# Kernel tuning notes

Measured on AMD Instinct MI355X. Metric: run time of the kernel, lower is better.

Reference implementation:

```python
import jax, jax.numpy as jnp
import numpy as np

H = 512   # embedding_dim (forced by Attention(512,512))
F = 21    # n_features
T = 28    # output_length

def _cell(x, h, c, Wih, Whh, b):
    # PyTorch LSTMCell math, gate order i,f,g,o
    g = x @ Wih.T + h @ Whh.T + b
    i, f, gg, o = jnp.split(g, 4, axis=-1)
    c2 = jax.nn.sigmoid(f) * c + jax.nn.sigmoid(i) * jnp.tanh(gg)
    h2 = jax.nn.sigmoid(o) * jnp.tanh(c2)
    return h2, c2

def _lstm3(inp, h, c, Wih0, Wih1, Wih2, Whh, bih, bhh):
    # 3-layer LSTM, single time step. h,c: [3,1,H]
    Wihs = (Wih0, Wih1, Wih2)
    hs, cs = [], []
    x = inp
    for l in range(3):
        hl, cl = _cell(x, h[l], c[l], Wihs[l], Whh[l], bih[l] + bhh[l])
        hs.append(hl); cs.append(cl)
        x = hl
    return x, jnp.stack(hs), jnp.stack(cs)

def setup_inputs() -> dict:
    key = jax.random.key(0)
    ks = jax.random.split(key, 20)
    s = 0.05
    f32 = jnp.float32
    return {
        "x": jax.random.normal(ks[0], (1, F), f32),
        "prev_y": jax.random.normal(ks[1], (1, F), f32),
        "enc_Wih0": jax.random.normal(ks[2], (4*H, F), f32) * s,
        "enc_Wih1": jax.random.normal(ks[3], (4*H, H), f32) * s,
        "enc_Wih2": jax.random.normal(ks[4], (4*H, H), f32) * s,
        "enc_Whh": jax.random.normal(ks[5], (3, 4*H, H), f32) * s,
        "enc_bih": jax.random.normal(ks[6], (3, 4*H), f32) * s,
        "enc_bhh": jax.random.normal(ks[7], (3, 4*H), f32) * s,
        "attn_W": jax.random.normal(ks[8], (H, 2*H), f32) * s,
        "attn_b": jax.random.normal(ks[9], (H,), f32) * s,
        "v_W": jax.random.normal(ks[10], (1, H), f32) * s,
        "dec_Wih0": jax.random.normal(ks[11], (4*H, H+F), f32) * s,
        "dec_Wih1": jax.random.normal(ks[12], (4*H, H), f32) * s,
        "dec_Wih2": jax.random.normal(ks[13], (4*H, H), f32) * s,
        "dec_Whh": jax.random.normal(ks[14], (3, 4*H, H), f32) * s,
        "dec_bih": jax.random.normal(ks[15], (3, 4*H), f32) * s,
        "dec_bhh": jax.random.normal(ks[16], (3, 4*H), f32) * s,
        "out_W": jax.random.normal(ks[17], (F, 2*H), f32) * s,
        "out_b": jax.random.normal(ks[18], (F,), f32) * s,
    }

def reference(x, prev_y, enc_Wih0, enc_Wih1, enc_Wih2, enc_Whh, enc_bih, enc_bhh,
              attn_W, attn_b, v_W, dec_Wih0, dec_Wih1, dec_Wih2, dec_Whh, dec_bih, dec_bhh,
              out_W, out_b):
    z = jnp.zeros((3, 1, H), x.dtype)
    # Encoder: single time step over feature-as-sequence input [1, F]
    enc_out, h, c = _lstm3(x, z, z, enc_Wih0, enc_Wih1, enc_Wih2, enc_Whh, enc_bih, enc_bhh)
    # enc_out: [1, H]; src_len == 1

    def step(carry, _):
        prev_out, h, c = carry
        # Bahdanau attention (src_len = 1)
        cat = jnp.concatenate([h[2], enc_out], axis=-1)          # [1, 2H]
        energy = jnp.tanh(cat @ attn_W.T + attn_b)               # [1, H]
        score = energy @ v_W.T                                    # [1, 1]
        a = jax.nn.softmax(score, axis=1)                         # [1, 1] (== 1)
        weighted = a * enc_out                                    # [1, H]
        rnn_in = jnp.concatenate([prev_out, weighted], axis=-1)  # [1, H+F]
        out, h2, c2 = _lstm3(rnn_in, h, c, dec_Wih0, dec_Wih1, dec_Wih2, dec_Whh, dec_bih, dec_bhh)
        y = jnp.concatenate([out, weighted], axis=-1) @ out_W.T + out_b  # [1, F]
        return (y, h2, c2), y

    _, ys = jax.lax.scan(step, (prev_y, h, c), None, length=T)
    return ys  # [T, 1, F]
```

## Files before the change

### kernel.cpp

```cpp
#include <hip/hip_runtime.h>
#include <cstddef>

constexpr int H  = 512;
constexpr int F  = 21;
constexpr int T  = 28;
constexpr int PB = 128;
constexpr int NB = PB + 1;
constexpr int NT = 256;
constexpr int NW = NT / 64;
constexpr int KR = 4;
constexpr int PH = 3 + 3 * T;

#define SCOPE_AGENT __HIP_MEMORY_SCOPE_AGENT

__device__ float g_hs[KR][2][PH][H];
__device__ unsigned g_epoch;

__device__ __forceinline__ int phS0(int t) { return 3 + 3 * t; }
__device__ __forceinline__ int phS1(int t) { return 4 + 3 * t; }
__device__ __forceinline__ int phS2(int t) { return 5 + 3 * t; }

struct P {
  const float *x, *py, *eW0, *eW1, *eW2, *ebih, *ebhh;
  const float *dW0, *dW1, *dW2, *dWhh, *dbih, *dbhh, *outW, *outb;
  float* out;
};

__device__ __forceinline__ float sigm(float v)  { return 1.0f / (1.0f + __expf(-v)); }
__device__ __forceinline__ float tanh_f(float v){ return 1.0f - 2.0f / (__expf(2.0f * v) + 1.0f); }

__device__ __forceinline__ float4 wredsum4(float4 v) {
#pragma unroll
  for (int off = 32; off > 0; off >>= 1) {
    v.x += __shfl_xor(v.x, off, 64);
    v.y += __shfl_xor(v.y, off, 64);
    v.z += __shfl_xor(v.z, off, 64);
    v.w += __shfl_xor(v.w, off, 64);
  }
  return v;
}
__device__ __forceinline__ float wredsum1(float v) {
#pragma unroll
  for (int off = 32; off > 0; off >>= 1) v += __shfl_xor(v, off, 64);
  return v;
}

__device__ __forceinline__ void pput4(int par, int ph, int r, float v) {
#pragma unroll
  for (int k = 0; k < KR; ++k)
    __hip_atomic_store(&g_hs[k][par][ph][r], v, __ATOMIC_RELAXED, SCOPE_AGENT);
}

__device__ __forceinline__ void stagev(const float* __restrict__ A,
                                       float* __restrict__ dst) {
  const int i = threadIdx.x;
  const unsigned long long* q = (const unsigned long long*)A + i;
  unsigned long long v = __hip_atomic_load(q, __ATOMIC_RELAXED, SCOPE_AGENT);
  int guard = 0;
  while (((unsigned)v == 0u || (unsigned)(v >> 32) == 0u) &&
         ++guard < (1 << 20)) {
    v = __hip_atomic_load(q, __ATOMIC_RELAXED, SCOPE_AGENT);
  }
  *(float2*)(dst + 2 * i) =
      make_float2(__uint_as_float((unsigned)v), __uint_as_float((unsigned)(v >> 32)));
  __syncthreads();
}

struct W8 { float4 a[4]; float4 b[4]; };

__device__ __forceinline__ W8 ldw_g(const float* __restrict__ W, int r, int lane) {
  W8 o;
#pragma unroll
  for (int g = 0; g < 4; ++g) {
    const float* q = W + (size_t)(g * H + r) * H + lane * 8;
    o.a[g] = *(const float4*)q;
    o.b[g] = *(const float4*)(q + 4);
  }
  return o;
}
__device__ __forceinline__ W8 ldw_lds(const float* sM, int w, int lane) {
  W8 o;
#pragma unroll
  for (int g = 0; g < 4; ++g) {
    const float* q = sM + (w * 4 + g) * H + lane * 8;
    o.a[g] = *(const float4*)q;
    o.b[g] = *(const float4*)(q + 4);
  }
  return o;
}
__device__ __forceinline__ void fma8(const W8& wt, const float4& x0, const float4& x1,
                                     float s[4]) {
#pragma unroll
  for (int g = 0; g < 4; ++g) {
    s[g] += wt.a[g].x * x0.x + wt.a[g].y * x0.y + wt.a[g].z * x0.z + wt.a[g].w * x0.w
          + wt.b[g].x * x1.x + wt.b[g].y * x1.y + wt.b[g].z * x1.z + wt.b[g].w * x1.w;
  }
}

__device__ __forceinline__ float cellup(const float4& v, const float b[4], float& c) {
  float cn = sigm(v.y + b[1]) * c + sigm(v.x + b[0]) * tanh_f(v.z + b[2]);
  c = cn;
  return sigm(v.w + b[3]) * tanh_f(cn);
}

__device__ __forceinline__ void write_y_frag(const P& p, int trow, int w, int lane,
                                             const float4& h0, const float4& h1,
                                             const float* sYe) {
  for (int j = w; j < F; j += NW) {
    const float* q = p.outW + (size_t)j * (2 * H) + lane * 8;
    float4 w0 = *(const float4*)q;
    float4 w1 = *(const float4*)(q + 4);
    float s = w0.x * h0.x + w0.y * h0.y + w0.z * h0.z + w0.w * h0.w
            + w1.x * h1.x + w1.y * h1.y + w1.z * h1.z + w1.w * h1.w;
    s = wredsum1(s);
    if (lane == 0) p.out[trow * F + j] = s + sYe[j];
  }
}

__global__ __launch_bounds__(NT, 1)
void k_flow(P p) {
  const int lane = threadIdx.x & 63;
  const int w    = threadIdx.x >> 6;
  const int sh   = blockIdx.x & (KR - 1);
  const unsigned ep =
      __hip_atomic_load(&g_epoch, __ATOMIC_RELAXED, SCOPE_AGENT);
  const int par = (int)(ep & 1u);

  __shared__ float sM[NW * 4 * H];
  __shared__ float sBuf[2][H];
  __shared__ float senc[H];
  __shared__ float sYe[F + 3];

  if (blockIdx.x == PB) {
    stagev(g_hs[sh][par][2], senc);
    {
      float4 e0 = *(const float4*)(senc + lane * 8);
      float4 e1 = *(const float4*)(senc + lane * 8 + 4);
      for (int j = w; j < F; j += NW) {
        const float* q = p.outW + (size_t)j * (2 * H) + H + lane * 8;
        float4 w0 = *(const float4*)q;
        float4 w1 = *(const float4*)(q + 4);
        float s = w0.x * e0.x + w0.y * e0.y + w0.z * e0.z + w0.w * e0.w
                + w1.x * e1.x + w1.y * e1.y + w1.z * e1.z + w1.w * e1.w;
        s = wredsum1(s);
        if (lane == 0) sYe[j] = s + p.outb[j];
      }
      __syncthreads();
    }
    for (int t = 0; t < T; ++t) {
      float* xb = sBuf[t & 1];
      stagev(g_hs[sh][par][phS2(t)], xb);
      float4 h20 = *(const float4*)(xb + lane * 8);
      float4 h21 = *(const float4*)(xb + lane * 8 + 4);
      write_y_frag(p, t, w, lane, h20, h21, sYe);
    }
    if (threadIdx.x == 0)
      __hip_atomic_fetch_add(&g_epoch, 1u, __ATOMIC_RELAXED, SCOPE_AGENT);
  } else {
    const int r = blockIdx.x * NW + w;

    float c0 = 0.f, c1 = 0.f, c2 = 0.f;
    float b00[4], b0p[4], b1s[4], b2s[4];
    float sOld0[4] = {0, 0, 0, 0}, sOld1[4] = {0, 0, 0, 0}, sOld2[4] = {0, 0, 0, 0};
    int bi = 0;

    {
      float s0 = 0.f, s1 = 0.f, s2 = 0.f, s3 = 0.f;
      if (lane < F) {
        const float xv = p.x[lane];
        s0 = p.eW0[(size_t)(0 * H + r) * F + lane] * xv;
        s1 = p.eW0[(size_t)(1 * H + r) * F + lane] * xv;
        s2 = p.eW0[(size_t)(2 * H + r) * F + lane] * xv;
        s3 = p.eW0[(size_t)(3 * H + r) * F + lane] * xv;
      }
      float4 v = wredsum4(make_float4(s0, s1, s2, s3));
      if (lane == 0) {
        const float* bi_ = p.ebih + r;
        const float* bh_ = p.ebhh + r;
        float cn = sigm(v.x + bi_[0] + bh_[0]) * tanh_f(v.z + bi_[2 * H] + bh_[2 * H]);
        c0 = cn;
        pput4(par, 0, r, sigm(v.w + bi_[3 * H] + bh_[3 * H]) * tanh_f(cn));
      }
    }

    {
      float4 mA[4], mB[4];
#pragma unroll
      for (int g = 0; g < 4; ++g) {
        mA[g] = make_float4(0.f, 0.f, 0.f, 0.f);
        mB[g] = make_float4(0.f, 0.f, 0.f, 0.f);
      }
      for (int f = 0; f < F; ++f) {
        const float* q = p.outW + (size_t)f * (2 * H) + lane * 8;
        const float4 oa = *(const float4*)q;
        const float4 ob = *(const float4*)(q + 4);
#pragma unroll
        for (int g = 0; g < 4; ++g) {
          const float wf = p.dW0[(size_t)(g * H + r) * (H + F) + f];
          mA[g].x += wf * oa.x; mA[g].y += wf * oa.y; mA[g].z += wf * oa.z; mA[g].w += wf * oa.w;
          mB[g].x += wf * ob.x; mB[g].y += wf * ob.y; mB[g].z += wf * ob.z; mB[g].w += wf * ob.w;
        }
      }
#pragma unroll
      for (int g = 0; g < 4; ++g) {
        *(float4*)(sM + (w * 4 + g) * H + lane * 8)     = mA[g];
        *(float4*)(sM + (w * 4 + g) * H + lane * 8 + 4) = mB[g];
      }
    }
#pragma unroll
    for (int g = 0; g < 4; ++g) {
      b1s[g] = p.dbih[4 * H + g * H + r] + p.dbhh[4 * H + g * H + r];
      b2s[g] = p.dbih[8 * H + g * H + r] + p.dbhh[8 * H + g * H + r];
    }

    {
      W8 wt = ldw_g(p.eW1, r, lane);
      stagev(g_hs[sh][par][0], sBuf[0]);
      float4 a0 = *(const float4*)(sBuf[0] + lane * 8);
      float4 a1 = *(const float4*)(sBuf[0] + lane * 8 + 4);
      float s[4] = {0.f, 0.f, 0.f, 0.f};
      fma8(wt, a0, a1, s);
      float4 v = wredsum4(make_float4(s[0], s[1], s[2], s[3]));
      if (lane == 0) {
        const float* bi_ = p.ebih + 4 * H + r;
        const float* bh_ = p.ebhh + 4 * H + r;
        float cn = sigm(v.x + bi_[0] + bh_[0]) * tanh_f(v.z + bi_[2 * H] + bh_[2 * H]);
        c1 = cn;
        pput4(par, 1, r, sigm(v.w + bi_[3 * H] + bh_[3 * H]) * tanh_f(cn));
      }
    }

    {
      W8 wt  = ldw_g(p.eW2, r, lane);
      W8 wh1 = ldw_g(p.dWhh + (size_t)4 * H * H, r, lane);
      stagev(g_hs[sh][par][1], sBuf[1]);
      float4 a0 = *(const float4*)(sBuf[1] + lane * 8);
      float4 a1 = *(const float4*)(sBuf[1] + lane * 8 + 4);
      float s[4] = {0.f, 0.f, 0.f, 0.f};
      fma8(wt, a0, a1, s);
      float4 v = wredsum4(make_float4(s[0], s[1], s[2], s[3]));
      if (lane == 0) {
        const float* bi_ = p.ebih + 8 * H + r;
        const float* bh_ = p.ebhh + 8 * H + r;
        float cn = sigm(v.x + bi_[0] + bh_[0]) * tanh_f(v.z + bi_[2 * H] + bh_[2 * H]);
        c2 = cn;
        pput4(par, 2, r, sigm(v.w + bi_[3 * H] + bh_[3 * H]) * tanh_f(cn));
      }
      fma8(wh1, a0, a1, sOld1);
    }

    {
      W8 wh2 = ldw_g(p.dWhh + (size_t)8 * H * H, r, lane);
      stagev(g_hs[sh][par][2], senc);
      float4 e0 = *(const float4*)(senc + lane * 8);
      float4 e1 = *(const float4*)(senc + lane * 8 + 4);
      for (int j = w; j < F; j += NW) {
        const float* q = p.outW + (size_t)j * (2 * H) + H + lane * 8;
        float4 w0 = *(const float4*)q;
        float4 w1 = *(const float4*)(q + 4);
        float s = w0.x * e0.x + w0.y * e0.y + w0.z * e0.z + w0.w * e0.w
                + w1.x * e1.x + w1.y * e1.y + w1.z * e1.z + w1.w * e1.w;
        s = wredsum1(s);
        if (lane == 0) sYe[j] = s + p.outb[j];
      }
      {
        float sg[4];
#pragma unroll
        for (int g = 0; g < 4; ++g) {
          const float* q = p.dW0 + (size_t)(g * H + r) * (H + F) + F + lane * 8;
          sg[g] = q[0] * e0.x + q[1] * e0.y + q[2] * e0.z + q[3] * e0.w
                + q[4] * e1.x + q[5] * e1.y + q[6] * e1.z + q[7] * e1.w;
        }
        float4 v = wredsum4(make_float4(sg[0], sg[1], sg[2], sg[3]));
        if (lane == 0) {
          b0p[0] = v.x + p.dbih[0 * H + r] + p.dbhh[0 * H + r];
          b0p[1] = v.y + p.dbih[1 * H + r] + p.dbhh[1 * H + r];
          b0p[2] = v.z + p.dbih[2 * H + r] + p.dbhh[2 * H + r];
          b0p[3] = v.w + p.dbih[3 * H + r] + p.dbhh[3 * H + r];
        }
      }
      {
        float f0 = 0.f, f1 = 0.f, f2 = 0.f, f3 = 0.f;
        if (lane < F) {
          const float yv = p.py[lane];
          f0 = p.dW0[(size_t)(0 * H + r) * (H + F) + lane] * yv;
          f1 = p.dW0[(size_t)(1 * H + r) * (H + F) + lane] * yv;
          f2 = p.dW0[(size_t)(2 * H + r) * (H + F) + lane] * yv;
          f3 = p.dW0[(size_t)(3 * H + r) * (H + F) + lane] * yv;
        }
        float4 v = wredsum4(make_float4(f0, f1, f2, f3));
        if (lane == 0) {
          b00[0] = b0p[0] + v.x; b00[1] = b0p[1] + v.y;
          b00[2] = b0p[2] + v.z; b00[3] = b0p[3] + v.w;
        }
      }
      __syncthreads();
      {
        float f0 = 0.f, f1 = 0.f, f2 = 0.f, f3 = 0.f;
        if (lane < F) {
          const float yv = sYe[lane];
          f0 = p.dW0[(size_t)(0 * H + r) * (H + F) + lane] * yv;
          f1 = p.dW0[(size_t)(1 * H + r) * (H + F) + lane] * yv;
          f2 = p.dW0[(size_t)(2 * H + r) * (H + F) + lane] * yv;
          f3 = p.dW0[(size_t)(3 * H + r) * (H + F) + lane] * yv;
        }
        float4 v = wredsum4(make_float4(f0, f1, f2, f3));
        if (lane == 0) {
          b0p[0] += v.x; b0p[1] += v.y; b0p[2] += v.z; b0p[3] += v.w;
        }
      }
      fma8(wh2, e0, e1, sOld2);
    }

    {
      W8 wh0 = ldw_g(p.dWhh, r, lane);
      float4 a0 = *(const float4*)(sBuf[0] + lane * 8);
      float4 a1 = *(const float4*)(sBuf[0] + lane * 8 + 4);
      float s[4] = {0.f, 0.f, 0.f, 0.f};
      fma8(wh0, a0, a1, s);
      float4 v = wredsum4(make_float4(s[0], s[1], s[2], s[3]));
      if (lane == 0) pput4(par, phS0(0), r, cellup(v, b00, c0));
    }
    __syncthreads();

    for (int t = 0; t < T; ++t) {
      if (t >= 1) {
        W8 wh2 = ldw_g(p.dWhh + (size_t)8 * H * H, r, lane);
        stagev(g_hs[sh][par][phS2(t - 1)], sBuf[bi]);
        W8 wm = ldw_lds(sM, w, lane);
        float4 h20 = *(const float4*)(sBuf[bi] + lane * 8);
        float4 h21 = *(const float4*)(sBuf[bi] + lane * 8 + 4);
        float s[4] = {sOld0[0], sOld0[1], sOld0[2], sOld0[3]};
        fma8(wm, h20, h21, s);
        float4 v = wredsum4(make_float4(s[0], s[1], s[2], s[3]));
        if (lane == 0) pput4(par, phS0(t), r, cellup(v, b0p, c0));
        sOld2[0] = sOld2[1] = sOld2[2] = sOld2[3] = 0.f;
        fma8(wh2, h20, h21, sOld2);
        bi ^= 1;
      }

      {
        W8 wi  = ldw_g(p.dW1, r, lane);
        W8 wh0 = ldw_g(p.dWhh, r, lane);
        stagev(g_hs[sh][par][phS0(t)], sBuf[bi]);
        float4 a0 = *(const float4*)(sBuf[bi] + lane * 8);
        float4 a1 = *(const float4*)(sBuf[bi] + lane * 8 + 4);
        float s[4] = {sOld1[0], sOld1[1], sOld1[2], sOld1[3]};
        fma8(wi, a0, a1, s);
        float4 v = wredsum4(make_float4(s[0], s[1], s[2], s[3]));
        if (lane == 0) pput4(par, phS1(t), r, cellup(v, b1s, c1));
        sOld0[0] = sOld0[1] = sOld0[2] = sOld0[3] = 0.f;
        fma8(wh0, a0, a1, sOld0);
        bi ^= 1;
      }
      {
        W8 wi  = ldw_g(p.dW2, r, lane);
        W8 wh1 = ldw_g(p.dWhh + (size_t)4 * H * H, r, lane);
        stagev(g_hs[sh][par][phS1(t)], sBuf[bi]);
        float4 a0 = *(const float4*)(sBuf[bi] + lane * 8);
        float4 a1 = *(const float4*)(sBuf[bi] + lane * 8 + 4);
        float s[4] = {sOld2[0], sOld2[1], sOld2[2], sOld2[3]};
        fma8(wi, a0, a1, s);
        float4 v = wredsum4(make_float4(s[0], s[1], s[2], s[3]));
        if (lane == 0) pput4(par, phS2(t), r, cellup(v, b2s, c2));
        sOld1[0] = sOld1[1] = sOld1[2] = sOld1[3] = 0.f;
        fma8(wh1, a0, a1, sOld1);
        bi ^= 1;
      }
    }

    {
      const int r0 = blockIdx.x * NW;
      const float4 z4 = make_float4(0.f, 0.f, 0.f, 0.f);
      for (int idx = threadIdx.x; idx < KR * PH; idx += NT)
        *(float4*)&g_hs[idx / PH][par ^ 1][idx % PH][r0] = z4;
    }
  }
}

extern "C" void kernel_launch(void* const* d_in, const int* in_sizes, int n_in,
                              void* d_out, int out_size, void* d_ws, size_t ws_size,
                              hipStream_t stream) {
  P p;
  p.x    = (const float*)d_in[0];
  p.py   = (const float*)d_in[1];
  p.eW0  = (const float*)d_in[2];
  p.eW1  = (const float*)d_in[3];
  p.eW2  = (const float*)d_in[4];
  p.ebih = (const float*)d_in[6];
  p.ebhh = (const float*)d_in[7];
  p.dW0  = (const float*)d_in[11];
  p.dW1  = (const float*)d_in[12];
  p.dW2  = (const float*)d_in[13];
  p.dWhh = (const float*)d_in[14];
  p.dbih = (const float*)d_in[15];
  p.dbhh = (const float*)d_in[16];
  p.outW = (const float*)d_in[17];
  p.outb = (const float*)d_in[18];
  p.out  = (float*)d_out;

  hipLaunchKernelGGL(k_flow, dim3(NB), dim3(NT), 0, stream, p);
}
```

Before: 306.7 us.

## Poll hidden-state vectors per wave with inline vector loads instead of block-staged LDS

Replaces the block-wide staging of each published hidden vector (per-thread 8-byte atomic polls into LDS followed by __syncthreads) with a per-wave poll. Each lane issues two global_load_dwordx4 with sc1 directly into registers and spins until all eight values are nonzero. This removes the LDS round trip and block barriers on the recurrent critical path, so each wave proceeds independently. Replica selection now uses the per-wave row index to spread polling across the KR copies. The cost is that every wave polls the full 2 KB vector on its own, which adds L2 traffic, and correctness depends on the sc1 cache-bypass semantics and the 16-byte alignment of g_hs.

```diff
diff --git a/kernel.cpp b/kernel.cpp
--- a/kernel.cpp
+++ b/kernel.cpp
@@ -13,7 +13,7 @@
 
 #define SCOPE_AGENT __HIP_MEMORY_SCOPE_AGENT
 
-__device__ float g_hs[KR][2][PH][H];
+__device__ __align__(16) float g_hs[KR][2][PH][H];
 __device__ unsigned g_epoch;
 
 __device__ __forceinline__ int phS0(int t) { return 3 + 3 * t; }
@@ -51,19 +51,26 @@
     __hip_atomic_store(&g_hs[k][par][ph][r], v, __ATOMIC_RELAXED, SCOPE_AGENT);
 }
 
-__device__ __forceinline__ void stagev(const float* __restrict__ A,
-                                       float* __restrict__ dst) {
-  const int i = threadIdx.x;
-  const unsigned long long* q = (const unsigned long long*)A + i;
-  unsigned long long v = __hip_atomic_load(q, __ATOMIC_RELAXED, SCOPE_AGENT);
+typedef unsigned int u32x4 __attribute__((ext_vector_type(4)));
+
+__device__ __forceinline__ void poll8(const float* __restrict__ A, int lane,
+                                      float4& x0, float4& x1) {
+  const float* q = A + lane * 8;
+  u32x4 a, b;
   int guard = 0;
-  while (((unsigned)v == 0u || (unsigned)(v >> 32) == 0u) &&
-         ++guard < (1 << 20)) {
-    v = __hip_atomic_load(q, __ATOMIC_RELAXED, SCOPE_AGENT);
-  }
-  *(float2*)(dst + 2 * i) =
-      make_float2(__uint_as_float((unsigned)v), __uint_as_float((unsigned)(v >> 32)));
-  __syncthreads();
+  bool bad;
+  do {
+    asm volatile("global_load_dwordx4 %0, %2, off sc1\n\t"
+                 "global_load_dwordx4 %1, %2, off offset:16 sc1\n\t"
+                 "s_waitcnt vmcnt(0)"
+                 : "=v"(a), "=v"(b) : "v"(q) : "memory");
+    bad = (a.x == 0u) | (a.y == 0u) | (a.z == 0u) | (a.w == 0u) |
+          (b.x == 0u) | (b.y == 0u) | (b.z == 0u) | (b.w == 0u);
+  } while (bad && ++guard < (1 << 20));
+  x0 = make_float4(__uint_as_float(a.x), __uint_as_float(a.y),
+                   __uint_as_float(a.z), __uint_as_float(a.w));
+  x1 = make_float4(__uint_as_float(b.x), __uint_as_float(b.y),
+                   __uint_as_float(b.z), __uint_as_float(b.w));
 }
 
 struct W8 { float4 a[4]; float4 b[4]; };
@@ -121,37 +128,30 @@
 void k_flow(P p) {
   const int lane = threadIdx.x & 63;
   const int w    = threadIdx.x >> 6;
-  const int sh   = blockIdx.x & (KR - 1);
+  const int sh   = (blockIdx.x * NW + w) & (KR - 1);
   const unsigned ep =
       __hip_atomic_load(&g_epoch, __ATOMIC_RELAXED, SCOPE_AGENT);
   const int par = (int)(ep & 1u);
 
   __shared__ float sM[NW * 4 * H];
-  __shared__ float sBuf[2][H];
-  __shared__ float senc[H];
   __shared__ float sYe[F + 3];
 
   if (blockIdx.x == PB) {
-    stagev(g_hs[sh][par][2], senc);
-    {
-      float4 e0 = *(const float4*)(senc + lane * 8);
-      float4 e1 = *(const float4*)(senc + lane * 8 + 4);
-      for (int j = w; j < F; j += NW) {
-        const float* q = p.outW + (size_t)j * (2 * H) + H + lane * 8;
-        float4 w0 = *(const float4*)q;
-        float4 w1 = *(const float4*)(q + 4);
-        float s = w0.x * e0.x + w0.y * e0.y + w0.z * e0.z + w0.w * e0.w
-                + w1.x * e1.x + w1.y * e1.y + w1.z * e1.z + w1.w * e1.w;
-        s = wredsum1(s);
-        if (lane == 0) sYe[j] = s + p.outb[j];
-      }
-      __syncthreads();
-    }
+    float4 e0, e1;
+    poll8(g_hs[sh][par][2], lane, e0, e1);
+    for (int j = w; j < F; j += NW) {
+      const float* q = p.outW + (size_t)j * (2 * H) + H + lane * 8;
+      float4 w0 = *(const float4*)q;
+      float4 w1 = *(const float4*)(q + 4);
+      float s = w0.x * e0.x + w0.y * e0.y + w0.z * e0.z + w0.w * e0.w
+              + w1.x * e1.x + w1.y * e1.y + w1.z * e1.z + w1.w * e1.w;
+      s = wredsum1(s);
+      if (lane == 0) sYe[j] = s + p.outb[j];
+    }
+    __syncthreads();
     for (int t = 0; t < T; ++t) {
-      float* xb = sBuf[t & 1];
-      stagev(g_hs[sh][par][phS2(t)], xb);
-      float4 h20 = *(const float4*)(xb + lane * 8);
-      float4 h21 = *(const float4*)(xb + lane * 8 + 4);
+      float4 h20, h21;
+      poll8(g_hs[sh][par][phS2(t)], lane, h20, h21);
       write_y_frag(p, t, w, lane, h20, h21, sYe);
     }
     if (threadIdx.x == 0)
@@ -162,7 +162,6 @@
     float c0 = 0.f, c1 = 0.f, c2 = 0.f;
     float b00[4], b0p[4], b1s[4], b2s[4];
     float sOld0[4] = {0, 0, 0, 0}, sOld1[4] = {0, 0, 0, 0}, sOld2[4] = {0, 0, 0, 0};
-    int bi = 0;
 
     {
       float s0 = 0.f, s1 = 0.f, s2 = 0.f, s3 = 0.f;
@@ -213,13 +212,12 @@
       b2s[g] = p.dbih[8 * H + g * H + r] + p.dbhh[8 * H + g * H + r];
     }
 
+    float4 aE0, aE1;
     {
       W8 wt = ldw_g(p.eW1, r, lane);
-      stagev(g_hs[sh][par][0], sBuf[0]);
-      float4 a0 = *(const float4*)(sBuf[0] + lane * 8);
-      float4 a1 = *(const float4*)(sBuf[0] + lane * 8 + 4);
+      poll8(g_hs[sh][par][0], lane, aE0, aE1);
       float s[4] = {0.f, 0.f, 0.f, 0.f};
-      fma8(wt, a0, a1, s);
+      fma8(wt, aE0, aE1, s);
       float4 v = wredsum4(make_float4(s[0], s[1], s[2], s[3]));
       if (lane == 0) {
         const float* bi_ = p.ebih + 4 * H + r;
@@ -233,9 +231,8 @@
     {
       W8 wt  = ldw_g(p.eW2, r, lane);
       W8 wh1 = ldw_g(p.dWhh + (size_t)4 * H * H, r, lane);
-      stagev(g_hs[sh][par][1], sBuf[1]);
-      float4 a0 = *(const float4*)(sBuf[1] + lane * 8);
-      float4 a1 = *(const float4*)(sBuf[1] + lane * 8 + 4);
+      float4 a0, a1;
+      poll8(g_hs[sh][par][1], lane, a0, a1);
       float s[4] = {0.f, 0.f, 0.f, 0.f};
       fma8(wt, a0, a1, s);
       float4 v = wredsum4(make_float4(s[0], s[1], s[2], s[3]));
@@ -251,9 +248,8 @@
 
     {
       W8 wh2 = ldw_g(p.dWhh + (size_t)8 * H * H, r, lane);
-      stagev(g_hs[sh][par][2], senc);
-      float4 e0 = *(const float4*)(senc + lane * 8);
-      float4 e1 = *(const float4*)(senc + lane * 8 + 4);
+      float4 e0, e1;
+      poll8(g_hs[sh][par][2], lane, e0, e1);
       for (int j = w; j < F; j += NW) {
         const float* q = p.outW + (size_t)j * (2 * H) + H + lane * 8;
         float4 w0 = *(const float4*)q;
@@ -314,58 +310,47 @@
 
     {
       W8 wh0 = ldw_g(p.dWhh, r, lane);
-      float4 a0 = *(const float4*)(sBuf[0] + lane * 8);
-      float4 a1 = *(const float4*)(sBuf[0] + lane * 8 + 4);
       float s[4] = {0.f, 0.f, 0.f, 0.f};
-      fma8(wh0, a0, a1, s);
+      fma8(wh0, aE0, aE1, s);
       float4 v = wredsum4(make_float4(s[0], s[1], s[2], s[3]));
       if (lane == 0) pput4(par, phS0(0), r, cellup(v, b00, c0));
     }
-    __syncthreads();
 
     for (int t = 0; t < T; ++t) {
+      float4 a0, a1;
       if (t >= 1) {
         W8 wh2 = ldw_g(p.dWhh + (size_t)8 * H * H, r, lane);
-        stagev(g_hs[sh][par][phS2(t - 1)], sBuf[bi]);
+        poll8(g_hs[sh][par][phS2(t - 1)], lane, a0, a1);
         W8 wm = ldw_lds(sM, w, lane);
-        float4 h20 = *(const float4*)(sBuf[bi] + lane * 8);
-        float4 h21 = *(const float4*)(sBuf[bi] + lane * 8 + 4);
         float s[4] = {sOld0[0], sOld0[1], sOld0[2], sOld0[3]};
-        fma8(wm, h20, h21, s);
+        fma8(wm, a0, a1, s);
         float4 v = wredsum4(make_float4(s[0], s[1], s[2], s[3]));
         if (lane == 0) pput4(par, phS0(t), r, cellup(v, b0p, c0));
         sOld2[0] = sOld2[1] = sOld2[2] = sOld2[3] = 0.f;
-        fma8(wh2, h20, h21, sOld2);
-        bi ^= 1;
+        fma8(wh2, a0, a1, sOld2);
       }
 
       {
         W8 wi  = ldw_g(p.dW1, r, lane);
         W8 wh0 = ldw_g(p.dWhh, r, lane);
-        stagev(g_hs[sh][par][phS0(t)], sBuf[bi]);
-        float4 a0 = *(const float4*)(sBuf[bi] + lane * 8);
-        float4 a1 = *(const float4*)(sBuf[bi] + lane * 8 + 4);
+        poll8(g_hs[sh][par][phS0(t)], lane, a0, a1);
         float s[4] = {sOld1[0], sOld1[1], sOld1[2], sOld1[3]};
         fma8(wi, a0, a1, s);
         float4 v = wredsum4(make_float4(s[0], s[1], s[2], s[3]));
         if (lane == 0) pput4(par, phS1(t), r, cellup(v, b1s, c1));
         sOld0[0] = sOld0[1] = sOld0[2] = sOld0[3] = 0.f;
         fma8(wh0, a0, a1, sOld0);
-        bi ^= 1;
       }
       {
         W8 wi  = ldw_g(p.dW2, r, lane);
         W8 wh1 = ldw_g(p.dWhh + (size_t)4 * H * H, r, lane);
-        stagev(g_hs[sh][par][phS1(t)], sBuf[bi]);
-        float4 a0 = *(const float4*)(sBuf[bi] + lane * 8);
-        float4 a1 = *(const float4*)(sBuf[bi] + lane * 8 + 4);
+        poll8(g_hs[sh][par][phS1(t)], lane, a0, a1);
         float s[4] = {sOld2[0], sOld2[1], sOld2[2], sOld2[3]};
         fma8(wi, a0, a1, s);
         float4 v = wredsum4(make_float4(s[0], s[1], s[2], s[3]));
         if (lane == 0) pput4(par, phS2(t), r, cellup(v, b2s, c2));
         sOld1[0] = sOld1[1] = sOld1[2] = sOld1[3] = 0.f;
         fma8(wh1, a0, a1, sOld1);
-        bi ^= 1;
       }
     }
 
```

Measured after the change: 512.4 us. +67.0%, slower.
